# Optimization experiments

Measured on AMD Instinct MI355X. Metric: run time of the kernel, lower is better.

The kernel has to match this reference:

```python
import jax, jax.numpy as jnp
import numpy as np

B, L, D, H, DH, DI, NL, V = 1, 2048, 1024, 16, 64, 4096, 12, 32000
EPS = 1e-5  # torch LayerNorm default eps
SCALE = 1.0 / DH ** 0.5


def _ln(x):
    # LayerNorm with elementwise_affine=False
    m = jnp.mean(x, axis=-1, keepdims=True)
    va = jnp.var(x, axis=-1, keepdims=True)
    return (x - m) / jnp.sqrt(va + EPS)


def setup_inputs() -> dict:
    key = jax.random.key(0)
    ks = jax.random.split(key, 12)
    s = 0.02
    return {
        "X": jax.random.randint(ks[0], (B, L), 0, V),
        "Y": jax.random.randint(ks[1], (B, L), 0, V),
        "emb": jax.random.normal(ks[2], (V, D), jnp.float32) * s,
        "u": jax.random.normal(ks[3], (H, DH), jnp.float32) * s,
        "v": jax.random.normal(ks[4], (H, DH), jnp.float32) * s,
        "Wqkv": jax.random.normal(ks[5], (NL, 3 * H * DH, D), jnp.float32) * s,
        "Wpe": jax.random.normal(ks[6], (NL, H * DH, D), jnp.float32) * s,
        "Wout": jax.random.normal(ks[7], (NL, D, H * DH), jnp.float32) * s,
        "W1": jax.random.normal(ks[8], (NL, DI, D), jnp.float32) * s,
        "b1": jnp.zeros((NL, DI), jnp.float32),
        "W2": jax.random.normal(ks[9], (NL, D, DI), jnp.float32) * s,
        "b2": jnp.zeros((NL, D), jnp.float32),
        "Wc": jax.random.normal(ks[10], (V, D), jnp.float32) * s,
        "bc": jnp.zeros((V,), jnp.float32),
    }


def _forward(X, emb, u, v, Wqkv, Wpe, Wout, W1, b1, W2, b2, Wc, bc):
    q_len = X.shape[1]
    k_len = q_len  # mems=None -> m_len=0
    h = emb[X]  # (B, L, D); d_embedding == d_model so no projection

    # sinusoidal relative position embedding over descending positions
    pos = jnp.arange(k_len - 1, -1, -1, dtype=h.dtype)
    inv_freq = 1.0 / (10000.0 ** (jnp.arange(0, D, 2, dtype=h.dtype) / D))
    pp = pos[:, None] * inv_freq[None, :]              # (k, D/2)
    pe = jnp.concatenate([jnp.sin(pp), jnp.cos(pp)], axis=1)[None]  # (1, k, D)

    # causal mask: triu(ones, diagonal=1 + m_len), m_len=0; True = masked
    mask = jnp.triu(jnp.ones((q_len, k_len), bool), k=1)

    def layer(hid, params):
        wqkv, wpe, wout, w1, bb1, w2, bb2 = params
        qkv = hid @ wqkv.T                              # (B, q, 3HD)
        Q, K, Vv = jnp.split(qkv, 3, axis=-1)
        Q = Q.reshape(B, q_len, H, DH)
        K = K.reshape(B, k_len, H, DH)
        Vv = Vv.reshape(B, k_len, H, DH)
        r = (pe @ wpe.T).reshape(B, k_len, H, DH)       # requires B == 1
        AC = jnp.einsum('bqhd,bkhd->bhqk', Q + u, K)
        # NOTE: original code calls relative_shift(BD) but DISCARDS the result,
        # so BD is used unshifted — we reproduce that faithfully.
        BD = jnp.einsum('bqhd,bkhd->bhqk', Q + v, r)
        score = (AC + BD) * SCALE
        score = jnp.where(mask[None, None], -jnp.inf, score)
        prob = jax.nn.softmax(score, axis=-1)
        av = jnp.einsum('bhqk,bkhd->bqhd', prob, Vv).reshape(B, q_len, H * DH)
        hid = _ln(hid + av @ wout.T)                    # post-norm attention
        ff = jax.nn.relu(hid @ w1.T + bb1) @ w2.T + bb2
        hid = _ln(hid + ff)                             # post-norm FFN
        return hid, None

    h, _ = jax.lax.scan(layer, h, (Wqkv, Wpe, Wout, W1, b1, W2, b2))
    logits = h @ Wc.T + bc                              # (B, L, V)
    return logits.reshape(B * q_len, V)


def reference(X, Y, emb, u, v, Wqkv, Wpe, Wout, W1, b1, W2, b2, Wc, bc):
    # Y only determines y_len; here y_len == q_len so the full hidden is used.
    return _forward(X, emb, u, v, Wqkv, Wpe, Wout, W1, b1, W2, b2, Wc, bc)
```

## Files before the change

kernel.cpp:

```cpp
#include <hip/hip_runtime.h>
#include <hip/hip_bf16.h>

#define L_ 2048
#define D_ 1024
#define H_ 16
#define DH_ 64
#define DI_ 4096
#define NL_ 12
#define V_ 32000
#define EPS_ 1e-5f
#define SCALE_ 0.125f
#define LOG2E_ 1.44269504f
#define KBLK 64

typedef __attribute__((ext_vector_type(8))) short short8;
typedef __attribute__((ext_vector_type(4))) float f32x4;
typedef __hip_bfloat16 bf16;

__device__ __forceinline__ void gload_lds16(const void* g, void* l) {
  __builtin_amdgcn_global_load_lds((const __attribute__((address_space(1))) void*)g,
                                   (__attribute__((address_space(3))) void*)l, 16, 0, 0);
}

template<int STORE_BF16, int BIAS, int RELU, int SPLITK>
__global__ __launch_bounds__(256)
void gemm_bt(const bf16* __restrict__ A, const bf16* __restrict__ B,
             void* __restrict__ C, const float* __restrict__ bias,
             int M, int N, int K, int lda, int ldb, int ldc,
             long long Astride, long long Bstride, long long Cstride,
             float alpha, int Kc)
{
  __shared__ __align__(16) bf16 Atile[2][128 * 32];
  __shared__ __align__(16) bf16 Btile[2][128 * 32];

  const int gx = gridDim.x;
  const int nwg = gx * gridDim.y;
  const int orig = blockIdx.x + gx * blockIdx.y;
  const int qq = nwg >> 3, rr = nwg & 7;
  const int xcd = orig & 7, sidx = orig >> 3;
  const int lin = (xcd < rr ? xcd * (qq + 1) : rr * (qq + 1) + (xcd - rr) * qq) + sidx;
  const int m0 = (lin % gx) * 128;
  const int n0 = (lin / gx) * 128;

  const int z = blockIdx.z;
  int kbeg, kend;
  const bf16 *Ab, *Bb;
  size_t czoff;
  if (SPLITK) {
    kbeg = z * Kc; kend = kbeg + Kc;
    Ab = A; Bb = B;
    czoff = (size_t)z * (size_t)Cstride;
  } else {
    kbeg = 0; kend = K;
    Ab = A + (size_t)z * (size_t)Astride;
    Bb = B + (size_t)z * (size_t)Bstride;
    czoff = (size_t)z * (size_t)Cstride;
  }

  const int t = threadIdx.x;
  const int lane = t & 63;
  const int w = t >> 6;
  const int wm = w >> 1;
  const int wn = w & 1;
  const int rl = lane & 15;
  const int kl = (lane >> 4) << 3;

  const int r0 = t >> 2, kk0 = (t & 3) << 3;
  const int r1 = (256 + t) >> 2, kk1 = ((256 + t) & 3) << 3;
  int rb0 = n0 + r0; if (rb0 >= N) rb0 = N - 1;
  int rb1 = n0 + r1; if (rb1 >= N) rb1 = N - 1;

  f32x4 zero = {0.f, 0.f, 0.f, 0.f};
  f32x4 acc[4][4];
#pragma unroll
  for (int i = 0; i < 4; ++i)
#pragma unroll
    for (int j = 0; j < 4; ++j) acc[i][j] = zero;

  auto stage = [&](int buf, int k0) {
    gload_lds16(Ab + (size_t)(m0 + r0) * lda + (k0 + kk0), Atile[buf] + w * 512);
    gload_lds16(Bb + (size_t)rb0 * ldb + (k0 + kk0),       Btile[buf] + w * 512);
    gload_lds16(Ab + (size_t)(m0 + r1) * lda + (k0 + kk1), Atile[buf] + 2048 + w * 512);
    gload_lds16(Bb + (size_t)rb1 * ldb + (k0 + kk1),       Btile[buf] + 2048 + w * 512);
  };

  stage(0, kbeg);
  __syncthreads();

  int cur = 0;
  for (int k0 = kbeg; k0 < kend; k0 += 32) {
    if (k0 + 32 < kend) stage(cur ^ 1, k0 + 32);

    short8 af[4], bf_[4];
#pragma unroll
    for (int fm = 0; fm < 4; ++fm)
      af[fm] = *(const short8*)(Atile[cur] + (wm * 64 + fm * 16 + rl) * 32 + kl);
#pragma unroll
    for (int fn = 0; fn < 4; ++fn)
      bf_[fn] = *(const short8*)(Btile[cur] + (wn * 64 + fn * 16 + rl) * 32 + kl);
#pragma unroll
    for (int fm = 0; fm < 4; ++fm)
#pragma unroll
      for (int fn = 0; fn < 4; ++fn)
        acc[fm][fn] = __builtin_amdgcn_mfma_f32_16x16x32_bf16(af[fm], bf_[fn], acc[fm][fn], 0, 0, 0);
    __syncthreads();
    cur ^= 1;
  }

  const int row_l = (lane >> 4) << 2;
  const int col_l = lane & 15;
#pragma unroll
  for (int fm = 0; fm < 4; ++fm) {
#pragma unroll
    for (int fn = 0; fn < 4; ++fn) {
#pragma unroll
      for (int j = 0; j < 4; ++j) {
        const int m = m0 + wm * 64 + fm * 16 + row_l + j;
        const int n = n0 + wn * 64 + fn * 16 + col_l;
        if (m < M && n < N) {
          float vv = acc[fm][fn][j] * alpha;
          if (BIAS) vv += bias[n];
          if (RELU) vv = fmaxf(vv, 0.f);
          if (STORE_BF16)
            ((bf16*)C)[czoff + (size_t)m * ldc + n] = __float2bfloat16(vv);
          else
            ((float*)C)[czoff + (size_t)m * ldc + n] = vv;
        }
      }
    }
  }
}

__global__ __launch_bounds__(256)
void attn_fused(const bf16* __restrict__ QuQv, const bf16* __restrict__ Kr,
                const bf16* __restrict__ VT, bf16* __restrict__ av)
{
  __shared__ __align__(16) bf16 Kt[KBLK * 128];
  __shared__ __align__(16) bf16 Vt[DH_ * KBLK];
  __shared__ __align__(16) bf16 Pt[4][16 * KBLK];

  const int bid = blockIdx.x;
  const int tile = (bid < 256) ? (31 - (bid >> 4)) : ((bid - 256) >> 4);
  const int head = bid & 15;
  const int q0 = tile * 64;
  const int t = threadIdx.x, lane = t & 63, w = t >> 6;
  const int rl = lane & 15, hi = lane >> 4;

  const bf16* Qh = QuQv + (size_t)head * L_ * 128;
  const bf16* Kh = Kr   + (size_t)head * L_ * 128;
  const bf16* Vh = VT   + (size_t)head * DH_ * L_;

  const int qw0 = q0 + w * 16;

  short8 qf[4];
#pragma unroll
  for (int ks = 0; ks < 4; ++ks)
    qf[ks] = *(const short8*)(Qh + (size_t)(qw0 + rl) * 128 + ks * 32 + hi * 8);

  f32x4 o[4];
  float m_r[4], l_r[4];
#pragma unroll
  for (int j = 0; j < 4; ++j) { m_r[j] = -INFINITY; l_r[j] = 0.f; }
#pragma unroll
  for (int fn = 0; fn < 4; ++fn) o[fn] = (f32x4){0.f, 0.f, 0.f, 0.f};

  short8 kreg[4], vreg[2];
  auto load_regs = [&](int k0) {
#pragma unroll
    for (int i = 0; i < 4; ++i) {
      int c = i * 256 + t;
      int row = c >> 4, d8 = (c & 15) << 3;
      kreg[i] = *(const short8*)(Kh + (size_t)(k0 + row) * 128 + d8);
    }
#pragma unroll
    for (int i = 0; i < 2; ++i) {
      int c = i * 256 + t;
      int d = c >> 3, k8 = (c & 7) << 3;
      vreg[i] = *(const short8*)(Vh + (size_t)d * L_ + k0 + k8);
    }
  };
  auto write_lds = [&]() {
#pragma unroll
    for (int i = 0; i < 4; ++i) {
      int c = i * 256 + t;
      int row = c >> 4, d8 = (c & 15) << 3;
      int off = (row << 8) + (((d8 << 1)) ^ ((row & 7) << 4));
      *(short8*)((char*)Kt + off) = kreg[i];
    }
#pragma unroll
    for (int i = 0; i < 2; ++i) {
      int c = i * 256 + t;
      int d = c >> 3, k8 = (c & 7) << 3;
      int off = (d << 7) + (((k8 << 1)) ^ ((d & 7) << 4));
      *(short8*)((char*)Vt + off) = vreg[i];
    }
  };

  load_regs(0);
  write_lds();
  __syncthreads();

  const int kend = q0 + 64;
  for (int k0 = 0; k0 < kend; k0 += KBLK) {
    const bool more = (k0 + KBLK) < kend;
    if (more) load_regs(k0 + KBLK);

    if (k0 <= qw0 + 15) {
      f32x4 s[4];
#pragma unroll
      for (int fn = 0; fn < 4; ++fn) s[fn] = (f32x4){0.f, 0.f, 0.f, 0.f};
      __builtin_amdgcn_s_setprio(1);
#pragma unroll
      for (int fn = 0; fn < 4; ++fn) {
        const int krow = fn * 16 + rl;
#pragma unroll
        for (int ks = 0; ks < 4; ++ks) {
          short8 kf = *(const short8*)((char*)Kt + (krow << 8) +
                        ((((ks * 32 + hi * 8) << 1)) ^ ((krow & 7) << 4)));
          s[fn] = __builtin_amdgcn_mfma_f32_16x16x32_bf16(qf[ks], kf, s[fn], 0, 0, 0);
        }
      }
      __builtin_amdgcn_s_setprio(0);
      if (k0 + KBLK > q0) {
#pragma unroll
        for (int fn = 0; fn < 4; ++fn) {
          const int key = k0 + fn * 16 + rl;
#pragma unroll
          for (int j = 0; j < 4; ++j)
            if (key > qw0 + hi * 4 + j) s[fn][j] = -1e30f;
        }
      }
      float mx[4];
#pragma unroll
      for (int j = 0; j < 4; ++j)
        mx[j] = fmaxf(fmaxf(s[0][j], s[1][j]), fmaxf(s[2][j], s[3][j]));
#pragma unroll
      for (int off = 1; off < 16; off <<= 1)
#pragma unroll
        for (int j = 0; j < 4; ++j) mx[j] = fmaxf(mx[j], __shfl_xor(mx[j], off));
      float sf[4];
#pragma unroll
      for (int j = 0; j < 4; ++j) {
        float mn = fmaxf(m_r[j], mx[j]);
        sf[j] = exp2f((m_r[j] - mn) * LOG2E_);
        m_r[j] = mn;
      }
      float rs[4] = {0.f, 0.f, 0.f, 0.f};
#pragma unroll
      for (int fn = 0; fn < 4; ++fn) {
#pragma unroll
        for (int j = 0; j < 4; ++j) {
          float p = exp2f((s[fn][j] - m_r[j]) * LOG2E_);
          rs[j] += p;
          int row = hi * 4 + j;
          *(bf16*)((char*)Pt[w] + (row << 7) +
                   ((((fn * 16 + rl) << 1)) ^ ((row & 7) << 4))) = __float2bfloat16(p);
        }
      }
#pragma unroll
      for (int off = 1; off < 16; off <<= 1)
#pragma unroll
        for (int j = 0; j < 4; ++j) rs[j] += __shfl_xor(rs[j], off);
#pragma unroll
      for (int j = 0; j < 4; ++j) l_r[j] = l_r[j] * sf[j] + rs[j];
#pragma unroll
      for (int fn = 0; fn < 4; ++fn)
#pragma unroll
        for (int j = 0; j < 4; ++j) o[fn][j] *= sf[j];

      __builtin_amdgcn_s_setprio(1);
#pragma unroll
      for (int ks2 = 0; ks2 < 2; ++ks2) {
        short8 pa = *(const short8*)((char*)Pt[w] + (rl << 7) +
                      ((ks2 * 64 + hi * 16) ^ ((rl & 7) << 4)));
#pragma unroll
        for (int fn = 0; fn < 4; ++fn) {
          const int drow = fn * 16 + rl;
          short8 vf = *(const short8*)((char*)Vt + (drow << 7) +
                        ((ks2 * 64 + hi * 16) ^ ((drow & 7) << 4)));
          o[fn] = __builtin_amdgcn_mfma_f32_16x16x32_bf16(pa, vf, o[fn], 0, 0, 0);
        }
      }
      __builtin_amdgcn_s_setprio(0);
    }

    if (more) {
      __syncthreads();
      write_lds();
      __syncthreads();
    }
  }

#pragma unroll
  for (int fn = 0; fn < 4; ++fn) {
#pragma unroll
    for (int j = 0; j < 4; ++j) {
      int q = qw0 + hi * 4 + j;
      float vv = o[fn][j] / l_r[j];
      av[(size_t)q * D_ + head * 64 + fn * 16 + rl] = __float2bfloat16(vv);
    }
  }
}

__global__ __launch_bounds__(256)
void embed_k(const int* __restrict__ X, const float* __restrict__ emb,
             float* __restrict__ hout, bf16* __restrict__ hbout)
{
  int idx = blockIdx.x * 256 + threadIdx.x;
  if (idx >= L_ * D_) return;
  int tpos = idx >> 10, d = idx & 1023;
  float vv = emb[(size_t)X[tpos] * D_ + d];
  hout[idx] = vv;
  hbout[idx] = __float2bfloat16(vv);
}

__global__ __launch_bounds__(256)
void pe_k(bf16* __restrict__ pe)
{
  int idx = blockIdx.x * 256 + threadIdx.x;
  if (idx >= L_ * D_) return;
  int k = idx >> 10, i = idx & 1023;
  int f = (i < 512) ? i : (i - 512);
  float invf = exp2f(-(float)(2 * f) * (13.28771238f / 1024.f));
  float pp = (float)(L_ - 1 - k) * invf;
  float vv = (i < 512) ? sinf(pp) : cosf(pp);
  pe[idx] = __float2bfloat16(vv);
}

__global__ __launch_bounds__(256)
void cast_all(const float* __restrict__ wqkv, const float* __restrict__ wpe,
              const float* __restrict__ wout, const float* __restrict__ w1,
              const float* __restrict__ w2,
              bf16* __restrict__ dqkv, bf16* __restrict__ dpe, bf16* __restrict__ dout,
              bf16* __restrict__ d1, bf16* __restrict__ d2)
{
  const int n4 = 13631488 / 4;
  for (int i = blockIdx.x * 256 + threadIdx.x; i < n4; i += gridDim.x * 256) {
    int j = i * 4;
    const float* src; bf16* dst; int o;
    if (j < 3145728)      { src = wqkv; dst = dqkv; o = j; }
    else if (j < 4194304) { src = wpe;  dst = dpe;  o = j - 3145728; }
    else if (j < 5242880) { src = wout; dst = dout; o = j - 4194304; }
    else if (j < 9437184) { src = w1;   dst = d1;   o = j - 5242880; }
    else                  { src = w2;   dst = d2;   o = j - 9437184; }
    float4 vv = *(const float4*)(src + o);
    dst[o + 0] = __float2bfloat16(vv.x);
    dst[o + 1] = __float2bfloat16(vv.y);
    dst[o + 2] = __float2bfloat16(vv.z);
    dst[o + 3] = __float2bfloat16(vv.w);
  }
}

__global__ __launch_bounds__(256)
void cast_bf4(const float* __restrict__ in, bf16* __restrict__ out, long long n4)
{
  for (long long i = (long long)blockIdx.x * 256 + threadIdx.x; i < n4; i += (long long)gridDim.x * 256) {
    float4 vv = *(const float4*)(in + i * 4);
    out[i * 4 + 0] = __float2bfloat16(vv.x);
    out[i * 4 + 1] = __float2bfloat16(vv.y);
    out[i * 4 + 2] = __float2bfloat16(vv.z);
    out[i * 4 + 3] = __float2bfloat16(vv.w);
  }
}

__global__ __launch_bounds__(256)
void split_qkv(const float* __restrict__ qkv, const float* __restrict__ r,
               const float* __restrict__ u, const float* __restrict__ v,
               bf16* __restrict__ QuQv, bf16* __restrict__ Kr)
{
  int idx = blockIdx.x * 256 + threadIdx.x;
  if (idx >= L_ * D_) return;
  int q = idx >> 10;
  int c = idx & 1023;
  int h = c >> 6;
  int d = c & 63;
  float Qv = qkv[(size_t)q * 3072 + c];
  float Kv = qkv[(size_t)q * 3072 + 1024 + c];
  float rr = r[idx] + r[(size_t)L_ * D_ + idx];
  size_t b = ((size_t)h * L_ + q) * 128;
  QuQv[b + d]      = __float2bfloat16((Qv + u[c]) * SCALE_);
  QuQv[b + 64 + d] = __float2bfloat16((Qv + v[c]) * SCALE_);
  Kr[b + d]        = __float2bfloat16(Kv);
  Kr[b + 64 + d]   = __float2bfloat16(rr);
}

__global__ __launch_bounds__(256)
void vtrans(const float* __restrict__ qkv, bf16* __restrict__ VT)
{
  __shared__ bf16 tile[64 * 65];
  const int q0 = blockIdx.x * 64;
  const int h = blockIdx.y;
  const int t = threadIdx.x;
  const int qi = t >> 4;
  const int d0 = (t & 15) * 4;
#pragma unroll
  for (int i = 0; i < 4; ++i) {
    int q = i * 16 + qi;
    float4 vv = *(const float4*)(qkv + (size_t)(q0 + q) * 3072 + 2048 + h * 64 + d0);
    tile[(d0 + 0) * 65 + q] = __float2bfloat16(vv.x);
    tile[(d0 + 1) * 65 + q] = __float2bfloat16(vv.y);
    tile[(d0 + 2) * 65 + q] = __float2bfloat16(vv.z);
    tile[(d0 + 3) * 65 + q] = __float2bfloat16(vv.w);
  }
  __syncthreads();
  const int dr = t >> 5;
  const int q2 = (t & 31) * 2;
#pragma unroll
  for (int i = 0; i < 8; ++i) {
    int dd = i * 8 + dr;
    __hip_bfloat162 pk;
    pk.x = tile[dd * 65 + q2];
    pk.y = tile[dd * 65 + q2 + 1];
    *(__hip_bfloat162*)(VT + ((size_t)h * 64 + dd) * L_ + q0 + q2) = pk;
  }
}

__global__ __launch_bounds__(256)
void ln_residual(const float* __restrict__ resid, const float* __restrict__ parts,
                 int nparts, long long pstride, const float* __restrict__ bias,
                 float* __restrict__ hout, bf16* __restrict__ hbout)
{
  const int row = blockIdx.x;
  const int t = threadIdx.x;
  const int lane = t & 63, w = t >> 6;
  const size_t base = (size_t)row * D_;
  __shared__ float rs[4], rs2[4];
  float4 xv = *(const float4*)(resid + base + t * 4);
  for (int p = 0; p < nparts; ++p) {
    float4 pv = *(const float4*)(parts + (size_t)p * pstride + base + t * 4);
    xv.x += pv.x; xv.y += pv.y; xv.z += pv.z; xv.w += pv.w;
  }
  if (bias) {
    float4 bv = *(const float4*)(bias + t * 4);
    xv.x += bv.x; xv.y += bv.y; xv.z += bv.z; xv.w += bv.w;
  }
  float s = xv.x + xv.y + xv.z + xv.w;
  float s2 = xv.x * xv.x + xv.y * xv.y + xv.z * xv.z + xv.w * xv.w;
#pragma unroll
  for (int off = 32; off; off >>= 1) {
    s += __shfl_down(s, off);
    s2 += __shfl_down(s2, off);
  }
  if (lane == 0) { rs[w] = s; rs2[w] = s2; }
  __syncthreads();
  float S = rs[0] + rs[1] + rs[2] + rs[3];
  float S2 = rs2[0] + rs2[1] + rs2[2] + rs2[3];
  float mean = S * (1.f / D_);
  float var = S2 * (1.f / D_) - mean * mean;
  float inv = 1.f / sqrtf(var + EPS_);
  float4 y;
  y.x = (xv.x - mean) * inv;
  y.y = (xv.y - mean) * inv;
  y.z = (xv.z - mean) * inv;
  y.w = (xv.w - mean) * inv;
  *(float4*)(hout + base + t * 4) = y;
  __hip_bfloat162 p0, p1;
  p0.x = __float2bfloat16(y.x); p0.y = __float2bfloat16(y.y);
  p1.x = __float2bfloat16(y.z); p1.y = __float2bfloat16(y.w);
  *(__hip_bfloat162*)(hbout + base + t * 4)     = p0;
  *(__hip_bfloat162*)(hbout + base + t * 4 + 2) = p1;
}

extern "C" void kernel_launch(void* const* d_in, const int* in_sizes, int n_in,
                              void* d_out, int out_size, void* d_ws, size_t ws_size,
                              hipStream_t stream)
{
  (void)in_sizes; (void)n_in; (void)out_size; (void)ws_size;
  const int*   X    = (const int*)d_in[0];
  const float* emb  = (const float*)d_in[2];
  const float* u    = (const float*)d_in[3];
  const float* v    = (const float*)d_in[4];
  const float* Wqkv = (const float*)d_in[5];
  const float* Wpe  = (const float*)d_in[6];
  const float* Wout = (const float*)d_in[7];
  const float* W1   = (const float*)d_in[8];
  const float* b1   = (const float*)d_in[9];
  const float* W2   = (const float*)d_in[10];
  const float* b2   = (const float*)d_in[11];
  const float* Wc   = (const float*)d_in[12];
  const float* bc   = (const float*)d_in[13];
  float* out = (float*)d_out;

  size_t off = 0;
  auto alloc = [&](size_t bytes) {
    void* p = (char*)d_ws + off;
    off += (bytes + 255) & ~(size_t)255;
    return p;
  };
  float* h_f32   = (float*)alloc((size_t)L_ * D_ * 4);
  bf16*  h_bf    = (bf16*) alloc((size_t)L_ * D_ * 2);
  bf16*  pe_bf   = (bf16*) alloc((size_t)L_ * D_ * 2);
  float* qkv_f   = (float*)alloc((size_t)L_ * 3 * D_ * 4);
  float* r_f     = (float*)alloc((size_t)2 * L_ * D_ * 4);
  bf16*  QuQv    = (bf16*) alloc((size_t)H_ * L_ * 128 * 2);
  bf16*  Kr      = (bf16*) alloc((size_t)H_ * L_ * 128 * 2);
  bf16*  VT      = (bf16*) alloc((size_t)H_ * DH_ * L_ * 2);
  bf16*  av_bf   = (bf16*) alloc((size_t)L_ * D_ * 2);
  float* part_f  = (float*)alloc((size_t)2 * L_ * D_ * 4);
  bf16*  ff1_bf  = (bf16*) alloc((size_t)L_ * DI_ * 2);
  bf16*  Wqkv_bf = (bf16*) alloc((size_t)3 * D_ * D_ * 2);
  bf16*  Wpe_bf  = (bf16*) alloc((size_t)D_ * D_ * 2);
  bf16*  Wout_bf = (bf16*) alloc((size_t)D_ * D_ * 2);
  bf16*  W1_bf   = (bf16*) alloc((size_t)DI_ * D_ * 2);
  bf16*  W2_bf   = (bf16*) alloc((size_t)D_ * DI_ * 2);
  bf16*  Wc_bf   = (bf16*) alloc((size_t)V_ * D_ * 2);

  const int eb = (L_ * D_ + 255) / 256;
  const long long LD = (long long)L_ * D_;

  embed_k<<<eb, 256, 0, stream>>>(X, emb, h_f32, h_bf);
  pe_k<<<eb, 256, 0, stream>>>(pe_bf);
  cast_bf4<<<2048, 256, 0, stream>>>(Wc, Wc_bf, (long long)V_ * D_ / 4);

  dim3 gqkv(L_ / 128, (3 * D_) / 128, 1);
  dim3 gsk (L_ / 128, D_ / 128, 2);
  dim3 gff1(L_ / 128, DI_ / 128, 1);

  for (int l = 0; l < NL_; ++l) {
    cast_all<<<2048, 256, 0, stream>>>(
        Wqkv + (size_t)l * 3 * D_ * D_, Wpe + (size_t)l * D_ * D_,
        Wout + (size_t)l * D_ * D_, W1 + (size_t)l * DI_ * D_, W2 + (size_t)l * D_ * DI_,
        Wqkv_bf, Wpe_bf, Wout_bf, W1_bf, W2_bf);

    gemm_bt<0, 0, 0, 0><<<gqkv, 256, 0, stream>>>(h_bf, Wqkv_bf, qkv_f, nullptr,
        L_, 3 * D_, D_, D_, D_, 3 * D_, 0, 0, 0, 1.f, 0);

    gemm_bt<0, 0, 0, 1><<<gsk, 256, 0, stream>>>(pe_bf, Wpe_bf, r_f, nullptr,
        L_, D_, D_, D_, D_, D_, 0, 0, LD, 1.f, 512);

    split_qkv<<<eb, 256, 0, stream>>>(qkv_f, r_f, u, v, QuQv, Kr);
    vtrans<<<dim3(L_ / 64, H_, 1), 256, 0, stream>>>(qkv_f, VT);

    attn_fused<<<512, 256, 0, stream>>>(QuQv, Kr, VT, av_bf);

    gemm_bt<0, 0, 0, 1><<<gsk, 256, 0, stream>>>(av_bf, Wout_bf, part_f, nullptr,
        L_, D_, D_, D_, D_, D_, 0, 0, LD, 1.f, 512);
    ln_residual<<<L_, 256, 0, stream>>>(h_f32, part_f, 2, LD, nullptr, h_f32, h_bf);

    gemm_bt<1, 1, 1, 0><<<gff1, 256, 0, stream>>>(h_bf, W1_bf, ff1_bf, b1 + (size_t)l * DI_,
        L_, DI_, D_, D_, D_, DI_, 0, 0, 0, 1.f, 0);

    gemm_bt<0, 0, 0, 1><<<gsk, 256, 0, stream>>>(ff1_bf, W2_bf, part_f, nullptr,
        L_, D_, DI_, DI_, DI_, D_, 0, 0, LD, 1.f, 2048);
    ln_residual<<<L_, 256, 0, stream>>>(h_f32, part_f, 2, LD, b2 + (size_t)l * D_, h_f32, h_bf);
  }

  dim3 gl(L_ / 128, V_ / 128, 1);
  gemm_bt<0, 1, 0, 0><<<gl, 256, 0, stream>>>(h_bf, Wc_bf, out, bc,
      L_, V_, D_, D_, D_, V_, 0, 0, 0, 1.f, 0);
}
```

Baseline: 3.279 ms.

## Read K/V fragments directly from global in attention; precast all layer weights upfront

The attention kernel drops its shared-memory K/V staging and block-wide barriers. Each wave now loads its K and V MFMA fragments straight from global memory, and only iterates up to its own causal bound. Separately, when the workspace is large enough, all layers' weights are cast to bf16 in a few large kernels before the layer loop, replacing one cast launch per layer. The attention change gives up shared-memory reuse across the four waves, so global/L2 traffic rises in exchange for removing the synchronisation. The precast path needs a much larger workspace and falls back to per-layer casts otherwise.

```diff
diff --git a/kernel.cpp b/kernel.cpp
--- a/kernel.cpp
+++ b/kernel.cpp
@@ -135,8 +135,6 @@
 void attn_fused(const bf16* __restrict__ QuQv, const bf16* __restrict__ Kr,
                 const bf16* __restrict__ VT, bf16* __restrict__ av)
 {
-  __shared__ __align__(16) bf16 Kt[KBLK * 128];
-  __shared__ __align__(16) bf16 Vt[DH_ * KBLK];
   __shared__ __align__(16) bf16 Pt[4][16 * KBLK];
 
   const int bid = blockIdx.x;
@@ -164,131 +162,90 @@
 #pragma unroll
   for (int fn = 0; fn < 4; ++fn) o[fn] = (f32x4){0.f, 0.f, 0.f, 0.f};
 
-  short8 kreg[4], vreg[2];
-  auto load_regs = [&](int k0) {
-#pragma unroll
-    for (int i = 0; i < 4; ++i) {
-      int c = i * 256 + t;
-      int row = c >> 4, d8 = (c & 15) << 3;
-      kreg[i] = *(const short8*)(Kh + (size_t)(k0 + row) * 128 + d8);
-    }
-#pragma unroll
-    for (int i = 0; i < 2; ++i) {
-      int c = i * 256 + t;
-      int d = c >> 3, k8 = (c & 7) << 3;
-      vreg[i] = *(const short8*)(Vh + (size_t)d * L_ + k0 + k8);
-    }
-  };
-  auto write_lds = [&]() {
-#pragma unroll
-    for (int i = 0; i < 4; ++i) {
-      int c = i * 256 + t;
-      int row = c >> 4, d8 = (c & 15) << 3;
-      int off = (row << 8) + (((d8 << 1)) ^ ((row & 7) << 4));
-      *(short8*)((char*)Kt + off) = kreg[i];
-    }
-#pragma unroll
-    for (int i = 0; i < 2; ++i) {
-      int c = i * 256 + t;
-      int d = c >> 3, k8 = (c & 7) << 3;
-      int off = (d << 7) + (((k8 << 1)) ^ ((d & 7) << 4));
-      *(short8*)((char*)Vt + off) = vreg[i];
-    }
-  };
-
-  load_regs(0);
-  write_lds();
-  __syncthreads();
-
-  const int kend = q0 + 64;
-  for (int k0 = 0; k0 < kend; k0 += KBLK) {
-    const bool more = (k0 + KBLK) < kend;
-    if (more) load_regs(k0 + KBLK);
-
-    if (k0 <= qw0 + 15) {
-      f32x4 s[4];
-#pragma unroll
-      for (int fn = 0; fn < 4; ++fn) s[fn] = (f32x4){0.f, 0.f, 0.f, 0.f};
-      __builtin_amdgcn_s_setprio(1);
+  const int kend_w = qw0 + 16;
+  for (int k0 = 0; k0 < kend_w; k0 += KBLK) {
+    short8 kf[4][4];
+#pragma unroll
+    for (int fn = 0; fn < 4; ++fn)
+#pragma unroll
+      for (int ks = 0; ks < 4; ++ks)
+        kf[fn][ks] = *(const short8*)(Kh + (size_t)(k0 + fn * 16 + rl) * 128 + ks * 32 + hi * 8);
+
+    f32x4 s[4];
+#pragma unroll
+    for (int fn = 0; fn < 4; ++fn) s[fn] = (f32x4){0.f, 0.f, 0.f, 0.f};
+    __builtin_amdgcn_s_setprio(1);
+#pragma unroll
+    for (int fn = 0; fn < 4; ++fn)
+#pragma unroll
+      for (int ks = 0; ks < 4; ++ks)
+        s[fn] = __builtin_amdgcn_mfma_f32_16x16x32_bf16(qf[ks], kf[fn][ks], s[fn], 0, 0, 0);
+    __builtin_amdgcn_s_setprio(0);
+
+    short8 vf[4][2];
+#pragma unroll
+    for (int fn = 0; fn < 4; ++fn)
+#pragma unroll
+      for (int ks2 = 0; ks2 < 2; ++ks2)
+        vf[fn][ks2] = *(const short8*)(Vh + (size_t)(fn * 16 + rl) * L_ + k0 + ks2 * 32 + hi * 8);
+
+    if (k0 + KBLK > q0) {
 #pragma unroll
       for (int fn = 0; fn < 4; ++fn) {
-        const int krow = fn * 16 + rl;
-#pragma unroll
-        for (int ks = 0; ks < 4; ++ks) {
-          short8 kf = *(const short8*)((char*)Kt + (krow << 8) +
-                        ((((ks * 32 + hi * 8) << 1)) ^ ((krow & 7) << 4)));
-          s[fn] = __builtin_amdgcn_mfma_f32_16x16x32_bf16(qf[ks], kf, s[fn], 0, 0, 0);
-        }
+        const int key = k0 + fn * 16 + rl;
+#pragma unroll
+        for (int j = 0; j < 4; ++j)
+          if (key > qw0 + hi * 4 + j) s[fn][j] = -1e30f;
       }
-      __builtin_amdgcn_s_setprio(0);
-      if (k0 + KBLK > q0) {
-#pragma unroll
-        for (int fn = 0; fn < 4; ++fn) {
-          const int key = k0 + fn * 16 + rl;
-#pragma unroll
-          for (int j = 0; j < 4; ++j)
-            if (key > qw0 + hi * 4 + j) s[fn][j] = -1e30f;
-        }
+    }
+    float mx[4];
+#pragma unroll
+    for (int j = 0; j < 4; ++j)
+      mx[j] = fmaxf(fmaxf(s[0][j], s[1][j]), fmaxf(s[2][j], s[3][j]));
+#pragma unroll
+    for (int off = 1; off < 16; off <<= 1)
+#pragma unroll
+      for (int j = 0; j < 4; ++j) mx[j] = fmaxf(mx[j], __shfl_xor(mx[j], off));
+    float sf[4];
+#pragma unroll
+    for (int j = 0; j < 4; ++j) {
+      float mn = fmaxf(m_r[j], mx[j]);
+      sf[j] = exp2f((m_r[j] - mn) * LOG2E_);
+      m_r[j] = mn;
+    }
+    float rs[4] = {0.f, 0.f, 0.f, 0.f};
+#pragma unroll
+    for (int fn = 0; fn < 4; ++fn) {
+#pragma unroll
+      for (int j = 0; j < 4; ++j) {
+        float p = exp2f((s[fn][j] - m_r[j]) * LOG2E_);
+        rs[j] += p;
+        int row = hi * 4 + j;
+        *(bf16*)((char*)Pt[w] + (row << 7) +
+                 ((((fn * 16 + rl) << 1)) ^ ((row & 7) << 4))) = __float2bfloat16(p);
       }
-      float mx[4];
-#pragma unroll
-      for (int j = 0; j < 4; ++j)
-        mx[j] = fmaxf(fmaxf(s[0][j], s[1][j]), fmaxf(s[2][j], s[3][j]));
-#pragma unroll
-      for (int off = 1; off < 16; off <<= 1)
-#pragma unroll
-        for (int j = 0; j < 4; ++j) mx[j] = fmaxf(mx[j], __shfl_xor(mx[j], off));
-      float sf[4];
-#pragma unroll
-      for (int j = 0; j < 4; ++j) {
-        float mn = fmaxf(m_r[j], mx[j]);
-        sf[j] = exp2f((m_r[j] - mn) * LOG2E_);
-        m_r[j] = mn;
-      }
-      float rs[4] = {0.f, 0.f, 0.f, 0.f};
-#pragma unroll
-      for (int fn = 0; fn < 4; ++fn) {
-#pragma unroll
-        for (int j = 0; j < 4; ++j) {
-          float p = exp2f((s[fn][j] - m_r[j]) * LOG2E_);
-          rs[j] += p;
-          int row = hi * 4 + j;
-          *(bf16*)((char*)Pt[w] + (row << 7) +
-                   ((((fn * 16 + rl) << 1)) ^ ((row & 7) << 4))) = __float2bfloat16(p);
-        }
-      }
-#pragma unroll
-      for (int off = 1; off < 16; off <<= 1)
-#pragma unroll
-        for (int j = 0; j < 4; ++j) rs[j] += __shfl_xor(rs[j], off);
-#pragma unroll
-      for (int j = 0; j < 4; ++j) l_r[j] = l_r[j] * sf[j] + rs[j];
+    }
+#pragma unroll
+    for (int off = 1; off < 16; off <<= 1)
+#pragma unroll
+      for (int j = 0; j < 4; ++j) rs[j] += __shfl_xor(rs[j], off);
+#pragma unroll
+    for (int j = 0; j < 4; ++j) l_r[j] = l_r[j] * sf[j] + rs[j];
+#pragma unroll
+    for (int fn = 0; fn < 4; ++fn)
+#pragma unroll
+      for (int j = 0; j < 4; ++j) o[fn][j] *= sf[j];
+
+    __builtin_amdgcn_s_setprio(1);
+#pragma unroll
+    for (int ks2 = 0; ks2 < 2; ++ks2) {
+      short8 pa = *(const short8*)((char*)Pt[w] + (rl << 7) +
+                    ((ks2 * 64 + hi * 16) ^ ((rl & 7) << 4)));
 #pragma unroll
       for (int fn = 0; fn < 4; ++fn)
-#pragma unroll
-        for (int j = 0; j < 4; ++j) o[fn][j] *= sf[j];
-
-      __builtin_amdgcn_s_setprio(1);
-#pragma unroll
-      for (int ks2 = 0; ks2 < 2; ++ks2) {
-        short8 pa = *(const short8*)((char*)Pt[w] + (rl << 7) +
-                      ((ks2 * 64 + hi * 16) ^ ((rl & 7) << 4)));
-#pragma unroll
-        for (int fn = 0; fn < 4; ++fn) {
-          const int drow = fn * 16 + rl;
-          short8 vf = *(const short8*)((char*)Vt + (drow << 7) +
-                        ((ks2 * 64 + hi * 16) ^ ((drow & 7) << 4)));
-          o[fn] = __builtin_amdgcn_mfma_f32_16x16x32_bf16(pa, vf, o[fn], 0, 0, 0);
-        }
-      }
-      __builtin_amdgcn_s_setprio(0);
-    }
-
-    if (more) {
-      __syncthreads();
-      write_lds();
-      __syncthreads();
-    }
+        o[fn] = __builtin_amdgcn_mfma_f32_16x16x32_bf16(pa, vf[fn][ks2], o[fn], 0, 0, 0);
+    }
+    __builtin_amdgcn_s_setprio(0);
   }
 
 #pragma unroll
@@ -465,7 +422,7 @@
                               void* d_out, int out_size, void* d_ws, size_t ws_size,
                               hipStream_t stream)
 {
-  (void)in_sizes; (void)n_in; (void)out_size; (void)ws_size;
+  (void)in_sizes; (void)n_in; (void)out_size;
   const int*   X    = (const int*)d_in[0];
   const float* emb  = (const float*)d_in[2];
   const float* u    = (const float*)d_in[3];
@@ -498,12 +455,17 @@
   bf16*  av_bf   = (bf16*) alloc((size_t)L_ * D_ * 2);
   float* part_f  = (float*)alloc((size_t)2 * L_ * D_ * 4);
   bf16*  ff1_bf  = (bf16*) alloc((size_t)L_ * DI_ * 2);
-  bf16*  Wqkv_bf = (bf16*) alloc((size_t)3 * D_ * D_ * 2);
-  bf16*  Wpe_bf  = (bf16*) alloc((size_t)D_ * D_ * 2);
-  bf16*  Wout_bf = (bf16*) alloc((size_t)D_ * D_ * 2);
-  bf16*  W1_bf   = (bf16*) alloc((size_t)DI_ * D_ * 2);
-  bf16*  W2_bf   = (bf16*) alloc((size_t)D_ * DI_ * 2);
   bf16*  Wc_bf   = (bf16*) alloc((size_t)V_ * D_ * 2);
+
+  const size_t perL = (size_t)(3 * D_ * D_ + D_ * D_ + D_ * D_ + DI_ * D_ + D_ * DI_) * 2;
+  size_t need_all = off + (size_t)NL_ * perL + 4096;
+  bool precast = (ws_size >= need_all);
+  int nlw = precast ? NL_ : 1;
+  bf16* Wqkv_bf = (bf16*)alloc((size_t)nlw * 3 * D_ * D_ * 2);
+  bf16* Wpe_bf  = (bf16*)alloc((size_t)nlw * D_ * D_ * 2);
+  bf16* Wout_bf = (bf16*)alloc((size_t)nlw * D_ * D_ * 2);
+  bf16* W1_bf   = (bf16*)alloc((size_t)nlw * DI_ * D_ * 2);
+  bf16* W2_bf   = (bf16*)alloc((size_t)nlw * D_ * DI_ * 2);
 
   const int eb = (L_ * D_ + 255) / 256;
   const long long LD = (long long)L_ * D_;
@@ -511,21 +473,36 @@
   embed_k<<<eb, 256, 0, stream>>>(X, emb, h_f32, h_bf);
   pe_k<<<eb, 256, 0, stream>>>(pe_bf);
   cast_bf4<<<2048, 256, 0, stream>>>(Wc, Wc_bf, (long long)V_ * D_ / 4);
+  if (precast) {
+    cast_bf4<<<2048, 256, 0, stream>>>(Wqkv, Wqkv_bf, (long long)NL_ * 3 * D_ * D_ / 4);
+    cast_bf4<<<2048, 256, 0, stream>>>(Wpe, Wpe_bf, (long long)NL_ * D_ * D_ / 4);
+    cast_bf4<<<2048, 256, 0, stream>>>(Wout, Wout_bf, (long long)NL_ * D_ * D_ / 4);
+    cast_bf4<<<2048, 256, 0, stream>>>(W1, W1_bf, (long long)NL_ * DI_ * D_ / 4);
+    cast_bf4<<<2048, 256, 0, stream>>>(W2, W2_bf, (long long)NL_ * D_ * DI_ / 4);
+  }
 
   dim3 gqkv(L_ / 128, (3 * D_) / 128, 1);
   dim3 gsk (L_ / 128, D_ / 128, 2);
   dim3 gff1(L_ / 128, DI_ / 128, 1);
 
   for (int l = 0; l < NL_; ++l) {
-    cast_all<<<2048, 256, 0, stream>>>(
-        Wqkv + (size_t)l * 3 * D_ * D_, Wpe + (size_t)l * D_ * D_,
-        Wout + (size_t)l * D_ * D_, W1 + (size_t)l * DI_ * D_, W2 + (size_t)l * D_ * DI_,
-        Wqkv_bf, Wpe_bf, Wout_bf, W1_bf, W2_bf);
-
-    gemm_bt<0, 0, 0, 0><<<gqkv, 256, 0, stream>>>(h_bf, Wqkv_bf, qkv_f, nullptr,
+    const int lw = precast ? l : 0;
+    bf16* wqkv_l = Wqkv_bf + (size_t)lw * 3 * D_ * D_;
+    bf16* wpe_l  = Wpe_bf  + (size_t)lw * D_ * D_;
+    bf16* wout_l = Wout_bf + (size_t)lw * D_ * D_;
+    bf16* w1_l   = W1_bf   + (size_t)lw * DI_ * D_;
+    bf16* w2_l   = W2_bf   + (size_t)lw * D_ * DI_;
+    if (!precast) {
+      cast_all<<<2048, 256, 0, stream>>>(
+          Wqkv + (size_t)l * 3 * D_ * D_, Wpe + (size_t)l * D_ * D_,
+          Wout + (size_t)l * D_ * D_, W1 + (size_t)l * DI_ * D_, W2 + (size_t)l * D_ * DI_,
+          wqkv_l, wpe_l, wout_l, w1_l, w2_l);
+    }
+
+    gemm_bt<0, 0, 0, 0><<<gqkv, 256, 0, stream>>>(h_bf, wqkv_l, qkv_f, nullptr,
         L_, 3 * D_, D_, D_, D_, 3 * D_, 0, 0, 0, 1.f, 0);
 
-    gemm_bt<0, 0, 0, 1><<<gsk, 256, 0, stream>>>(pe_bf, Wpe_bf, r_f, nullptr,
+    gemm_bt<0, 0, 0, 1><<<gsk, 256, 0, stream>>>(pe_bf, wpe_l, r_f, nullptr,
         L_, D_, D_, D_, D_, D_, 0, 0, LD, 1.f, 512);
 
     split_qkv<<<eb, 256, 0, stream>>>(qkv_f, r_f, u, v, QuQv, Kr);
@@ -533,14 +510,14 @@
 
     attn_fused<<<512, 256, 0, stream>>>(QuQv, Kr, VT, av_bf);
 
-    gemm_bt<0, 0, 0, 1><<<gsk, 256, 0, stream>>>(av_bf, Wout_bf, part_f, nullptr,
+    gemm_bt<0, 0, 0, 1><<<gsk, 256, 0, stream>>>(av_bf, wout_l, part_f, nullptr,
         L_, D_, D_, D_, D_, D_, 0, 0, LD, 1.f, 512);
     ln_residual<<<L_, 256, 0, stream>>>(h_f32, part_f, 2, LD, nullptr, h_f32, h_bf);
 
-    gemm_bt<1, 1, 1, 0><<<gff1, 256, 0, stream>>>(h_bf, W1_bf, ff1_bf, b1 + (size_t)l * DI_,
+    gemm_bt<1, 1, 1, 0><<<gff1, 256, 0, stream>>>(h_bf, w1_l, ff1_bf, b1 + (size_t)l * DI_,
         L_, DI_, D_, D_, D_, DI_, 0, 0, 0, 1.f, 0);
 
-    gemm_bt<0, 0, 0, 1><<<gsk, 256, 0, stream>>>(ff1_bf, W2_bf, part_f, nullptr,
+    gemm_bt<0, 0, 0, 1><<<gsk, 256, 0, stream>>>(ff1_bf, w2_l, part_f, nullptr,
         L_, D_, DI_, DI_, DI_, D_, 0, 0, LD, 1.f, 2048);
     ln_residual<<<L_, 256, 0, stream>>>(h_f32, part_f, 2, LD, b2 + (size_t)l * D_, h_f32, h_bf);
   }
```

Result: slower. 3.881 ms (+18.3%).
